# Optimization experiments

Measured on AMD Instinct MI355X. Metric: run time of the kernel, lower is better.

## Reference

```python
import jax, jax.numpy as jnp
import numpy as np

B, LQ, LK, H, A = 32, 2048, 2048, 1024, 512


def setup_inputs() -> dict:
    key = jax.random.key(0)
    ks = jax.random.split(key, 5)
    s = 1.0 / np.sqrt(H)
    return {
        "query": jax.random.normal(ks[0], (B, LQ, H), jnp.float32),
        "key": jax.random.normal(ks[1], (B, LK, H), jnp.float32),
        "Wq": jax.random.normal(ks[2], (H, A), jnp.float32) * s,
        "bq": jnp.zeros((A,), jnp.float32),
        "Wk": jax.random.normal(ks[3], (H, A), jnp.float32) * s,
        "bk": jnp.zeros((A,), jnp.float32),
        "Wv": jax.random.normal(ks[4], (A, 1), jnp.float32) * (1.0 / np.sqrt(A)),
        "bv": jnp.zeros((1,), jnp.float32),
    }


def reference(query, key, Wq, bq, Wk, bk, Wv, bv):
    # Linear projections
    Qp = jnp.einsum("bqh,ha->bqa", query, Wq) + bq          # [B, LQ, A]
    Kp = jnp.einsum("bkh,ha->bka", key, Wk) + bk            # [B, LK, A]
    # Score matrix Q(query) @ K(key)^T
    alpha_mat = jnp.einsum("bqa,bka->bqk", Qp, Kp)          # [B, LQ, LK]
    # Sum over query dim, softmax over key dim
    alpha = jax.nn.softmax(alpha_mat.sum(axis=1, keepdims=True), axis=2)  # [B, 1, LK]
    # Per-key scalar head V applied to projected keys, then weighted combine
    v = jnp.einsum("bka,ao->bko", Kp, Wv) + bv              # [B, LK, 1]
    x = jnp.matmul(alpha, v)[:, 0, :]                        # [B, 1]
    return x
```

## Files before the change

kernel.cpp:

```cpp
#include <hip/hip_runtime.h>
#include <math.h>

#define NB 32
#define LQ 2048
#define LK 2048
#define HD 1024
#define AD 512
#define QCH 64

typedef float vf4 __attribute__((ext_vector_type(4)));

__global__ void __launch_bounds__(256)
k1_stream(const float* __restrict__ query, const float* __restrict__ Wk,
          const float* __restrict__ Wv, const float* __restrict__ bk,
          const float* __restrict__ bv, float* __restrict__ partial,
          float* __restrict__ wv_eff, float* __restrict__ c_v) {
    const int bid = blockIdx.x;
    const int t = threadIdx.x;
    if (bid < NB * QCH) {
        int b = bid / QCH, qc = bid % QCH;
        const int QPC = LQ / QCH;
        vf4 a0 = {0.f,0.f,0.f,0.f}, a1 = {0.f,0.f,0.f,0.f};
        vf4 a2 = {0.f,0.f,0.f,0.f}, a3 = {0.f,0.f,0.f,0.f};
        const vf4* src = (const vf4*)(query + ((size_t)b * LQ + (size_t)qc * QPC) * HD);
        for (int q = 0; q < QPC; q += 4) {
            vf4 v0 = __builtin_nontemporal_load(&src[(size_t)(q + 0) * (HD / 4) + t]);
            vf4 v1 = __builtin_nontemporal_load(&src[(size_t)(q + 1) * (HD / 4) + t]);
            vf4 v2 = __builtin_nontemporal_load(&src[(size_t)(q + 2) * (HD / 4) + t]);
            vf4 v3 = __builtin_nontemporal_load(&src[(size_t)(q + 3) * (HD / 4) + t]);
            a0 += v0; a1 += v1; a2 += v2; a3 += v3;
        }
        vf4 acc = (a0 + a1) + (a2 + a3);
        ((vf4*)(partial + ((size_t)qc * NB + b) * HD))[t] = acc;
    } else if (bid < NB * QCH + 16) {
        int w = t >> 6, lane = t & 63;
        int gw = (bid - NB * QCH) * 4 + w;
        const float4* vv = (const float4*)Wv;
        for (int r = 0; r < 16; ++r) {
            int h = gw * 16 + r;
            const float4* wr = (const float4*)(Wk + (size_t)h * AD);
            double acc = 0.0;
            #pragma unroll
            for (int j = 0; j < 2; ++j) {
                int f = lane + 64 * j;
                float4 w4 = wr[f];
                float4 v4 = vv[f];
                acc += (double)w4.x * v4.x + (double)w4.y * v4.y
                     + (double)w4.z * v4.z + (double)w4.w * v4.w;
            }
            #pragma unroll
            for (int off = 32; off > 0; off >>= 1) acc += __shfl_down(acc, off);
            if (lane == 0) wv_eff[h] = (float)acc;
        }
    } else if (t < 64) {
        int lane = t;
        const float4* br = (const float4*)bk;
        const float4* vv = (const float4*)Wv;
        double acc = 0.0;
        #pragma unroll
        for (int j = 0; j < 2; ++j) {
            int f = lane + 64 * j;
            float4 b4 = br[f];
            float4 v4 = vv[f];
            acc += (double)b4.x * v4.x + (double)b4.y * v4.y
                 + (double)b4.z * v4.z + (double)b4.w * v4.w;
        }
        #pragma unroll
        for (int off = 32; off > 0; off >>= 1) acc += __shfl_down(acc, off);
        if (lane == 0) c_v[0] = (float)(acc + (double)bv[0]);
    }
}

__global__ void __launch_bounds__(256)
k2_qsum(const float* __restrict__ partial, const float* __restrict__ Wq,
        const float* __restrict__ bq, float* __restrict__ qsum) {
    __shared__ float sq[HD];
    __shared__ double red[4][64];
    int b = blockIdx.x >> 3;
    int a0 = (blockIdx.x & 7) * 64;
    int t = threadIdx.x;

    #pragma unroll
    for (int c = 0; c < 4; ++c) {
        int h = t + c * 256;
        float acc = 0.f;
        #pragma unroll 4
        for (int qc = 0; qc < QCH; ++qc)
            acc += partial[((size_t)qc * NB + b) * HD + h];
        sq[h] = acc;
    }
    __syncthreads();

    int w = t >> 6, lane = t & 63;
    int a = a0 + lane;
    const float* wp = Wq + a;
    double c0 = 0.0, c1 = 0.0, c2 = 0.0, c3 = 0.0;
    int hbase = w * 256;
    for (int i = 0; i < 256; i += 4) {
        int h = hbase + i;
        c0 += (double)sq[h]     * wp[(size_t)h * AD];
        c1 += (double)sq[h + 1] * wp[(size_t)(h + 1) * AD];
        c2 += (double)sq[h + 2] * wp[(size_t)(h + 2) * AD];
        c3 += (double)sq[h + 3] * wp[(size_t)(h + 3) * AD];
    }
    red[w][lane] = ((c0 + c1) + (c2 + c3));
    __syncthreads();
    if (t < 64) {
        double s = red[0][t] + red[1][t] + red[2][t] + red[3][t];
        qsum[(size_t)b * AD + a0 + t] = (float)(s + (double)LQ * bq[a0 + t]);
    }
}

__global__ void __launch_bounds__(256)
k3_weff(const float* __restrict__ qsum, const float* __restrict__ Wk,
        float* __restrict__ wk_eff) {
    int w = threadIdx.x >> 6, lane = threadIdx.x & 63;
    int widx = blockIdx.x * 4 + w;
    int base = widx * 4;
    for (int r = 0; r < 4; r += 2) {
        int idx0 = base + r;
        int b = idx0 >> 10, h0 = idx0 & (HD - 1);
        const float4* r0 = (const float4*)(Wk + (size_t)h0 * AD);
        const float4* r1 = (const float4*)(Wk + (size_t)(h0 + 1) * AD);
        const float4* qs = (const float4*)(qsum + (size_t)b * AD);
        double a0 = 0.0, a1 = 0.0;
        #pragma unroll
        for (int j = 0; j < 2; ++j) {
            int f = lane + 64 * j;
            float4 w0 = r0[f];
            float4 w1 = r1[f];
            float4 q4 = qs[f];
            a0 += (double)w0.x * q4.x + (double)w0.y * q4.y
                + (double)w0.z * q4.z + (double)w0.w * q4.w;
            a1 += (double)w1.x * q4.x + (double)w1.y * q4.y
                + (double)w1.z * q4.z + (double)w1.w * q4.w;
        }
        #pragma unroll
        for (int off = 32; off > 0; off >>= 1) {
            a0 += __shfl_down(a0, off);
            a1 += __shfl_down(a1, off);
        }
        if (lane == 0) {
            wk_eff[idx0]     = (float)a0;
            wk_eff[idx0 + 1] = (float)a1;
        }
    }
}

__global__ void __launch_bounds__(256)
k4_scores(const float* __restrict__ key, const float* __restrict__ wk_eff,
          const float* __restrict__ wv_eff, const float* __restrict__ c_v,
          float* __restrict__ scores, float* __restrict__ vvals) {
    __shared__ float lwk[HD];
    __shared__ float lwv[HD];
    const int bid = blockIdx.x;
    const int b = bid >> 6;
    const int k0 = (bid & 63) * 32;
    const int t = threadIdx.x;
    for (int i = t; i < HD; i += 256) {
        lwk[i] = wk_eff[(size_t)b * HD + i];
        lwv[i] = wv_eff[i];
    }
    __syncthreads();
    int w = t >> 6, lane = t & 63;
    double cv = (double)c_v[0];
    const vf4* lwk4 = (const vf4*)lwk;
    const vf4* lwv4 = (const vf4*)lwv;
    for (int rp = 0; rp < 2; ++rp) {
        int k = k0 + w * 8 + rp * 4;
        const vf4* kr0 = (const vf4*)(key + ((size_t)b * LK + k) * HD);
        const vf4* kr1 = kr0 + (HD / 4);
        const vf4* kr2 = kr0 + 2 * (HD / 4);
        const vf4* kr3 = kr0 + 3 * (HD / 4);
        double sc0 = 0.0, vv0 = 0.0, sc1 = 0.0, vv1 = 0.0;
        double sc2 = 0.0, vv2 = 0.0, sc3 = 0.0, vv3 = 0.0;
        #pragma unroll
        for (int j = 0; j < 4; ++j) {
            int f = lane + 64 * j;
            vf4 k0v = __builtin_nontemporal_load(&kr0[f]);
            vf4 k1v = __builtin_nontemporal_load(&kr1[f]);
            vf4 k2v = __builtin_nontemporal_load(&kr2[f]);
            vf4 k3v = __builtin_nontemporal_load(&kr3[f]);
            vf4 wk4 = lwk4[f];
            vf4 wv4 = lwv4[f];
            sc0 += (double)k0v[0] * wk4[0] + (double)k0v[1] * wk4[1]
                 + (double)k0v[2] * wk4[2] + (double)k0v[3] * wk4[3];
            vv0 += (double)k0v[0] * wv4[0] + (double)k0v[1] * wv4[1]
                 + (double)k0v[2] * wv4[2] + (double)k0v[3] * wv4[3];
            sc1 += (double)k1v[0] * wk4[0] + (double)k1v[1] * wk4[1]
                 + (double)k1v[2] * wk4[2] + (double)k1v[3] * wk4[3];
            vv1 += (double)k1v[0] * wv4[0] + (double)k1v[1] * wv4[1]
                 + (double)k1v[2] * wv4[2] + (double)k1v[3] * wv4[3];
            sc2 += (double)k2v[0] * wk4[0] + (double)k2v[1] * wk4[1]
                 + (double)k2v[2] * wk4[2] + (double)k2v[3] * wk4[3];
            vv2 += (double)k2v[0] * wv4[0] + (double)k2v[1] * wv4[1]
                 + (double)k2v[2] * wv4[2] + (double)k2v[3] * wv4[3];
            sc3 += (double)k3v[0] * wk4[0] + (double)k3v[1] * wk4[1]
                 + (double)k3v[2] * wk4[2] + (double)k3v[3] * wk4[3];
            vv3 += (double)k3v[0] * wv4[0] + (double)k3v[1] * wv4[1]
                 + (double)k3v[2] * wv4[2] + (double)k3v[3] * wv4[3];
        }
        #pragma unroll
        for (int off = 32; off > 0; off >>= 1) {
            sc0 += __shfl_down(sc0, off);
            vv0 += __shfl_down(vv0, off);
            sc1 += __shfl_down(sc1, off);
            vv1 += __shfl_down(vv1, off);
            sc2 += __shfl_down(sc2, off);
            vv2 += __shfl_down(vv2, off);
            sc3 += __shfl_down(sc3, off);
            vv3 += __shfl_down(vv3, off);
        }
        if (lane == 0) {
            size_t base = (size_t)b * LK + k;
            scores[base]     = (float)sc0;  vvals[base]     = (float)(vv0 + cv);
            scores[base + 1] = (float)sc1;  vvals[base + 1] = (float)(vv1 + cv);
            scores[base + 2] = (float)sc2;  vvals[base + 2] = (float)(vv2 + cv);
            scores[base + 3] = (float)sc3;  vvals[base + 3] = (float)(vv3 + cv);
        }
    }
}

__global__ void __launch_bounds__(256)
k5_softmax(const float* __restrict__ scores, const float* __restrict__ vvals,
           float* __restrict__ out) {
    int b = blockIdx.x;
    int t = threadIdx.x;
    __shared__ float smax_sh[4];
    __shared__ double num_sh[4], den_sh[4];
    const float* sr = scores + (size_t)b * LK;
    const float* vr = vvals  + (size_t)b * LK;
    float m = -INFINITY;
    for (int k = t; k < LK; k += 256) m = fmaxf(m, sr[k]);
    #pragma unroll
    for (int off = 32; off > 0; off >>= 1) m = fmaxf(m, __shfl_down(m, off));
    int w = t >> 6, lane = t & 63;
    if (lane == 0) smax_sh[w] = m;
    __syncthreads();
    float gm = fmaxf(fmaxf(smax_sh[0], smax_sh[1]), fmaxf(smax_sh[2], smax_sh[3]));
    double num = 0.0, den = 0.0;
    for (int k = t; k < LK; k += 256) {
        double e = exp((double)(sr[k] - gm));
        den += e;
        num += e * (double)vr[k];
    }
    #pragma unroll
    for (int off = 32; off > 0; off >>= 1) {
        num += __shfl_down(num, off);
        den += __shfl_down(den, off);
    }
    if (lane == 0) { num_sh[w] = num; den_sh[w] = den; }
    __syncthreads();
    if (t == 0) {
        double N = num_sh[0] + num_sh[1] + num_sh[2] + num_sh[3];
        double D = den_sh[0] + den_sh[1] + den_sh[2] + den_sh[3];
        out[b] = (float)(N / D);
    }
}

extern "C" void kernel_launch(void* const* d_in, const int* in_sizes, int n_in,
                              void* d_out, int out_size, void* d_ws, size_t ws_size,
                              hipStream_t stream) {
    const float* query = (const float*)d_in[0];
    const float* key   = (const float*)d_in[1];
    const float* Wq    = (const float*)d_in[2];
    const float* bq    = (const float*)d_in[3];
    const float* Wk    = (const float*)d_in[4];
    const float* bk    = (const float*)d_in[5];
    const float* Wv    = (const float*)d_in[6];
    const float* bv    = (const float*)d_in[7];
    float* out = (float*)d_out;

    float* ws = (float*)d_ws;
    size_t off = 0;
    float* partial = ws + off; off += (size_t)QCH * NB * HD;
    float* qsum    = ws + off; off += (size_t)NB * AD;
    float* wk_eff  = ws + off; off += (size_t)NB * HD;
    float* wv_eff  = ws + off; off += (size_t)HD;
    float* c_v     = ws + off; off += 1;
    float* scores  = ws + off; off += (size_t)NB * LK;
    float* vvals   = ws + off; off += (size_t)NB * LK;

    hipLaunchKernelGGL(k1_stream, dim3(NB * QCH + 16 + 1), dim3(256), 0, stream,
                       query, Wk, Wv, bk, bv, partial, wv_eff, c_v);
    hipLaunchKernelGGL(k2_qsum, dim3(256), dim3(256), 0, stream,
                       partial, Wq, bq, qsum);
    hipLaunchKernelGGL(k3_weff, dim3(2048), dim3(256), 0, stream,
                       qsum, Wk, wk_eff);
    hipLaunchKernelGGL(k4_scores, dim3(NB * (LK / 32)), dim3(256), 0, stream,
                       key, wk_eff, wv_eff, c_v, scores, vvals);
    hipLaunchKernelGGL(k5_softmax, dim3(NB), dim3(256), 0, stream,
                       scores, vvals, out);
}
```

Measured before the change: 146.9 us.

## Fuse qsum and wk_eff kernels into one mid-stage kernel

Merges the query-sum projection through Wq and the Wk-based effective weight computation into a single 512-thread kernel. The intermediate qsum is kept in shared memory instead of going through global memory, and one launch is dropped. In exchange, each block now recomputes the full 512-wide Wq projection for its batch (8x redundant across the 8 blocks per batch), so each block reads all of Wq. Only 256 blocks cover the Wk stage, down from 2048.

New measurement: 157.9 us. +7.5%, slower.

```diff
diff --git a/kernel.cpp b/kernel.cpp
--- a/kernel.cpp
+++ b/kernel.cpp
@@ -71,18 +71,19 @@
     }
 }
 
-__global__ void __launch_bounds__(256)
-k2_qsum(const float* __restrict__ partial, const float* __restrict__ Wq,
-        const float* __restrict__ bq, float* __restrict__ qsum) {
+__global__ void __launch_bounds__(512)
+kM_mid(const float* __restrict__ partial, const float* __restrict__ Wq,
+       const float* __restrict__ bq, const float* __restrict__ Wk,
+       float* __restrict__ wk_eff) {
     __shared__ float sq[HD];
-    __shared__ double red[4][64];
-    int b = blockIdx.x >> 3;
-    int a0 = (blockIdx.x & 7) * 64;
-    int t = threadIdx.x;
+    __shared__ float qs[AD];
+    const int bid = blockIdx.x;
+    const int b = bid >> 3, j = bid & 7;
+    const int t = threadIdx.x;
 
     #pragma unroll
-    for (int c = 0; c < 4; ++c) {
-        int h = t + c * 256;
+    for (int c = 0; c < 2; ++c) {
+        int h = t + c * 512;
         float acc = 0.f;
         #pragma unroll 4
         for (int qc = 0; qc < QCH; ++qc)
@@ -91,45 +92,33 @@
     }
     __syncthreads();
 
+    {
+        const float* wp = Wq + t;
+        double c0 = 0.0, c1 = 0.0, c2 = 0.0, c3 = 0.0;
+        for (int h = 0; h < HD; h += 4) {
+            c0 += (double)sq[h]     * wp[(size_t)h * AD];
+            c1 += (double)sq[h + 1] * wp[(size_t)(h + 1) * AD];
+            c2 += (double)sq[h + 2] * wp[(size_t)(h + 2) * AD];
+            c3 += (double)sq[h + 3] * wp[(size_t)(h + 3) * AD];
+        }
+        qs[t] = (float)(((c0 + c1) + (c2 + c3)) + (double)LQ * (double)bq[t]);
+    }
+    __syncthreads();
+
     int w = t >> 6, lane = t & 63;
-    int a = a0 + lane;
-    const float* wp = Wq + a;
-    double c0 = 0.0, c1 = 0.0, c2 = 0.0, c3 = 0.0;
-    int hbase = w * 256;
-    for (int i = 0; i < 256; i += 4) {
-        int h = hbase + i;
-        c0 += (double)sq[h]     * wp[(size_t)h * AD];
-        c1 += (double)sq[h + 1] * wp[(size_t)(h + 1) * AD];
-        c2 += (double)sq[h + 2] * wp[(size_t)(h + 2) * AD];
-        c3 += (double)sq[h + 3] * wp[(size_t)(h + 3) * AD];
-    }
-    red[w][lane] = ((c0 + c1) + (c2 + c3));
-    __syncthreads();
-    if (t < 64) {
-        double s = red[0][t] + red[1][t] + red[2][t] + red[3][t];
-        qsum[(size_t)b * AD + a0 + t] = (float)(s + (double)LQ * bq[a0 + t]);
-    }
-}
-
-__global__ void __launch_bounds__(256)
-k3_weff(const float* __restrict__ qsum, const float* __restrict__ Wk,
-        float* __restrict__ wk_eff) {
-    int w = threadIdx.x >> 6, lane = threadIdx.x & 63;
-    int widx = blockIdx.x * 4 + w;
-    int base = widx * 4;
-    for (int r = 0; r < 4; r += 2) {
-        int idx0 = base + r;
-        int b = idx0 >> 10, h0 = idx0 & (HD - 1);
+    const float4* qs4 = (const float4*)qs;
+    int h0base = j * 128 + w * 16;
+    for (int r = 0; r < 16; r += 2) {
+        int h0 = h0base + r;
         const float4* r0 = (const float4*)(Wk + (size_t)h0 * AD);
         const float4* r1 = (const float4*)(Wk + (size_t)(h0 + 1) * AD);
-        const float4* qs = (const float4*)(qsum + (size_t)b * AD);
         double a0 = 0.0, a1 = 0.0;
         #pragma unroll
-        for (int j = 0; j < 2; ++j) {
-            int f = lane + 64 * j;
+        for (int jj = 0; jj < 2; ++jj) {
+            int f = lane + 64 * jj;
             float4 w0 = r0[f];
             float4 w1 = r1[f];
-            float4 q4 = qs[f];
+            float4 q4 = qs4[f];
             a0 += (double)w0.x * q4.x + (double)w0.y * q4.y
                 + (double)w0.z * q4.z + (double)w0.w * q4.w;
             a1 += (double)w1.x * q4.x + (double)w1.y * q4.y
@@ -141,8 +130,8 @@
             a1 += __shfl_down(a1, off);
         }
         if (lane == 0) {
-            wk_eff[idx0]     = (float)a0;
-            wk_eff[idx0 + 1] = (float)a1;
+            wk_eff[(size_t)b * HD + h0]     = (float)a0;
+            wk_eff[(size_t)b * HD + h0 + 1] = (float)a1;
         }
     }
 }
@@ -175,8 +164,8 @@
         double sc0 = 0.0, vv0 = 0.0, sc1 = 0.0, vv1 = 0.0;
         double sc2 = 0.0, vv2 = 0.0, sc3 = 0.0, vv3 = 0.0;
         #pragma unroll
-        for (int j = 0; j < 4; ++j) {
-            int f = lane + 64 * j;
+        for (int jj = 0; jj < 4; ++jj) {
+            int f = lane + 64 * jj;
             vf4 k0v = __builtin_nontemporal_load(&kr0[f]);
             vf4 k1v = __builtin_nontemporal_load(&kr1[f]);
             vf4 k2v = __builtin_nontemporal_load(&kr2[f]);
@@ -274,7 +263,6 @@
     float* ws = (float*)d_ws;
     size_t off = 0;
     float* partial = ws + off; off += (size_t)QCH * NB * HD;
-    float* qsum    = ws + off; off += (size_t)NB * AD;
     float* wk_eff  = ws + off; off += (size_t)NB * HD;
     float* wv_eff  = ws + off; off += (size_t)HD;
     float* c_v     = ws + off; off += 1;
@@ -283,10 +271,8 @@
 
     hipLaunchKernelGGL(k1_stream, dim3(NB * QCH + 16 + 1), dim3(256), 0, stream,
                        query, Wk, Wv, bk, bv, partial, wv_eff, c_v);
-    hipLaunchKernelGGL(k2_qsum, dim3(256), dim3(256), 0, stream,
-                       partial, Wq, bq, qsum);
-    hipLaunchKernelGGL(k3_weff, dim3(2048), dim3(256), 0, stream,
-                       qsum, Wk, wk_eff);
+    hipLaunchKernelGGL(kM_mid, dim3(256), dim3(512), 0, stream,
+                       partial, Wq, bq, Wk, wk_eff);
     hipLaunchKernelGGL(k4_scores, dim3(NB * (LK / 32)), dim3(256), 0, stream,
                        key, wk_eff, wv_eff, c_v, scores, vvals);
     hipLaunchKernelGGL(k5_softmax, dim3(NB), dim3(256), 0, stream,
```
